# Kernel tuning notes

Hardware: AMD Instinct MI355X
Metric: run time of the kernel (lower is better)

The kernel has to match this reference:

```python
import jax, jax.numpy as jnp
import numpy as np

B = 256
H = W = 14
HW = H * W
TS = 0.03  # sigmoid temperature
TC = 0.07  # contrastive temperature
TP_K = int(HW * 0.1)   # 19
TN_K = int(HW * 0.5)   # 98
EPS_NORM = 1e-12
EPS_PD = 1e-6  # torch F.pairwise_distance eps


def _l2norm(x, axis):
    n = jnp.sqrt(jnp.sum(x * x, axis=axis, keepdims=True))
    return x / jnp.maximum(n, EPS_NORM)


def _conv(x, w):
    return jax.lax.conv_general_dilated(
        x, w, window_strides=(1, 1), padding='SAME',
        dimension_numbers=('NCHW', 'OIHW', 'NCHW'))


def setup_inputs() -> dict:
    key = jax.random.key(0)
    ks = jax.random.split(key, 7)
    ev = jax.random.normal(ks[0], (B, 384, H, W), dtype=jnp.float32)
    ea = jax.random.normal(ks[1], (B, 2048), dtype=jnp.float32)
    masks = jax.random.randint(ks[2], (B, H, W), 0, 2).astype(jnp.int32)
    masks = masks.at[:, 0, 0].set(1)  # guarantee nonzero mask area
    W_fc1 = jax.random.normal(ks[3], (512, 2048), dtype=jnp.float32) * 0.02
    W_fc2 = jax.random.normal(ks[4], (512, 512), dtype=jnp.float32) * 0.02
    W_conv1 = jax.random.normal(ks[5], (512, 384, 3, 3), dtype=jnp.float32) * 0.02
    W_conv2 = jax.random.normal(ks[6], (512, 512, 3, 3), dtype=jnp.float32) * 0.02
    return {'ev': ev, 'ea': ea, 'masks': masks, 'W_fc1': W_fc1,
            'W_fc2': W_fc2, 'W_conv1': W_conv1, 'W_conv2': W_conv2}


def reference(ev, ea, masks, W_fc1, W_fc2, W_conv1, W_conv2):
    # Audio_Proj: fc2(relu(fc1(ea)))  -> (B, 512)
    fa = jnp.maximum(ea @ W_fc1.T, 0.0) @ W_fc2.T

    # Visual_Proj: conv2(relu(conv1(ev))) -> (B, 512, 14, 14)
    fv_map = _conv(jnp.maximum(_conv(ev, W_conv1), 0.0), W_conv2)
    fv_map_norm = _l2norm(fv_map, axis=1)

    # masked mean pooling over the Ncut mask -> indicator vector (B, 512)
    m = masks.astype(jnp.float32)
    ind_vec = jnp.sum(fv_map * m[:, None], axis=(2, 3)) / jnp.sum(m, axis=(1, 2))[:, None]
    ind_vec_norm = _l2norm(ind_vec, axis=1)

    # Sij[i, j, p] = <fv_map_norm[i, :, p], ind_vec_norm[j]>  -> (B, B, HW)
    Sij = jnp.einsum('ichw,jc->ijhw', fv_map_norm, ind_vec_norm).reshape(B, B, HW)

    # per-row topk thresholds (kth largest / kth smallest)
    pos_thr = jax.lax.top_k(Sij, TP_K)[0][..., -1:]           # (B, B, 1)
    neg_thr = -jax.lax.top_k(-Sij, TN_K)[0][..., -1:]         # (B, B, 1)

    m_p = jax.nn.sigmoid((Sij - pos_thr) / TS)
    m_n = 1.0 - jax.nn.sigmoid((Sij - neg_thr) / TS)

    SP = jnp.sum(Sij * m_p, axis=-1) / jnp.sum(m_p, axis=-1)  # (B, B)
    SN = jnp.sum(Sij * m_n, axis=-1) / jnp.sum(m_n, axis=-1)  # (B, B)

    logits1 = jnp.concatenate([SP, SN], axis=1) / TC          # (B, 2B)
    logits2 = jnp.concatenate([SP.T, SN.T], axis=1) / TC
    labels = jnp.arange(B)
    loss1 = -jnp.mean(jax.nn.log_softmax(logits1, axis=-1)[labels, labels])
    loss2 = -jnp.mean(jax.nn.log_softmax(logits2, axis=-1)[labels, labels])

    # squared pairwise distance between detached ind_vec and fa (torch eps in diff)
    diff = jax.lax.stop_gradient(ind_vec)[:, None, :] - fa[None, :, :] + EPS_PD
    dist_mat = jnp.sum(diff * diff, axis=-1)                  # (B, B)

    ivn_d = jax.lax.stop_gradient(ind_vec_norm)
    vv_logits = ivn_d @ ivn_d.T
    eye = jnp.eye(B, dtype=jnp.float32)
    w = -vv_logits * (1.0 - eye) + eye
    dist_mat = dist_mat * w

    mask_mat = eye - (1.0 - eye) / (B - 1)
    loss3 = jnp.mean(jnp.maximum(jnp.sum(dist_mat * mask_mat, axis=1) + 0.6, 0.0))
    loss4 = jnp.mean(jnp.maximum(jnp.sum(dist_mat * mask_mat, axis=0) + 0.6, 0.0))

    return ((loss1 + loss2) / 2.0, (loss3 + loss4) / 2.0)
```

## Files before the change

kernel.cpp:

```cpp
#include <hip/hip_runtime.h>
#include <stdint.h>


typedef __attribute__((ext_vector_type(8))) short bf16x8;
typedef __attribute__((ext_vector_type(4))) short short4v;
typedef __attribute__((ext_vector_type(4))) float f32x4;

__device__ __forceinline__ unsigned short f2bf(float x) {
  unsigned u = __float_as_uint(x);
  unsigned r = u + 0x7FFFu + ((u >> 16) & 1u);
  return (unsigned short)(r >> 16);
}
__device__ __forceinline__ float bf2f(unsigned short h) {
  return __uint_as_float(((unsigned)h) << 16);
}

typedef const __attribute__((address_space(1))) void* gptr1_t;
typedef __attribute__((address_space(3))) void* lptr3_t;
__device__ __forceinline__ void gload_lds16(const void* g, void* l) {
  __builtin_amdgcn_global_load_lds((gptr1_t)g, (lptr3_t)l, 16, 0, 0);
}

__device__ __forceinline__ float waveSum(float v) {
#pragma unroll
  for (int m = 1; m < 64; m <<= 1) v += __shfl_xor(v, m, 64);
  return v;
}
__device__ __forceinline__ float waveMax(float v) {
#pragma unroll
  for (int m = 1; m < 64; m <<= 1) v = fmaxf(v, __shfl_xor(v, m, 64));
  return v;
}
template <int NW>
__device__ __forceinline__ float blockSum(float v) {
  __shared__ float sh[NW];
  v = waveSum(v);
  int wv = threadIdx.x >> 6, ln = threadIdx.x & 63;
  if (ln == 0) sh[wv] = v;
  __syncthreads();
  float r = 0.f;
#pragma unroll
  for (int w = 0; w < NW; ++w) r += sh[w];
  __syncthreads();
  return r;
}
template <int NW>
__device__ __forceinline__ float blockMax(float v) {
  __shared__ float sh[NW];
  v = waveMax(v);
  int wv = threadIdx.x >> 6, ln = threadIdx.x & 63;
  if (ln == 0) sh[wv] = v;
  __syncthreads();
  float r = -3.4e38f;
#pragma unroll
  for (int w = 0; w < NW; ++w) r = fmaxf(r, sh[w]);
  __syncthreads();
  return r;
}

#define RA 65536

template <int KC, int EPI>
__global__ __launch_bounds__(256, 2) void convtap6_k(
    const unsigned short* __restrict__ A, const unsigned short* __restrict__ Bw,
    unsigned short* __restrict__ C) {
  __shared__ __align__(16) short Ah[256 * 72];
  const int tid = threadIdx.x;
  const int wave = tid >> 6, lane = tid & 63;
  const int wm = wave >> 1, wn = wave & 1;
  const int quad = lane >> 4, tq = lane & 15;
  const int img = blockIdx.x, n0 = blockIdx.y * 128;

  int pab[7];
  {
    const int dh = tq >> 3;
    int wq = wm * 8 + (tq & 7);
    if (wq == 0) wq = 8;
    else if (wq == 15) wq = 7;
#pragma unroll
    for (int mi = 0; mi < 7; ++mi) {
      int pr = (1 + 2 * mi + dh) * 16 + wq;
      pab[mi] = (pr - 17) * 144 + quad * 16;
    }
  }
  const int gb = (n0 >> 4) + wn * 4;

  const char* Ab = (const char*)A;
  const char* AhB = (const char*)Ah;
  const int l16 = lane * 16;

  f32x4 acc[7][4];
#pragma unroll
  for (int mi = 0; mi < 7; ++mi)
#pragma unroll
    for (int ni = 0; ni < 4; ++ni) {
      f32x4 z = {0.f, 0.f, 0.f, 0.f};
      acc[mi][ni] = z;
    }

  auto stageA = [&](int kc) {
    size_t s0 = ((size_t)kc * RA + img * 256) * 144;
#pragma unroll
    for (int i = 0; i < 9; ++i) {
      int c = wave + i * 4;
      gload_lds16(Ab + s0 + (size_t)c * 1024 + l16, (char*)Ah + c * 1024);
    }
  };

  stageA(0);
  bf16x8 b0[4], b1[4];
  {
    const size_t w0 = ((size_t)gb * 128 + lane) * 8;
#pragma unroll
    for (int ni = 0; ni < 4; ++ni)
      b0[ni] = *(const bf16x8*)&Bw[w0 + (size_t)ni * 1024];
  }
  __syncthreads();

#pragma unroll 1
  for (int kc = 0; kc < KC; ++kc) {
    const size_t bk = ((size_t)kc * 4096 + gb * 128 + lane) * 8;
#pragma unroll
    for (int t = 0; t < 9; ++t) {
      const size_t tof = (size_t)t * KC * 32768;
#pragma unroll
      for (int ni = 0; ni < 4; ++ni)
        b1[ni] = *(const bf16x8*)&Bw[bk + tof + (size_t)ni * 1024 + 512];
      bf16x8 b0n[4];
      const bool last = (t == 8) && (kc == KC - 1);
      if (!last) {
        const size_t nbase =
            (t < 8) ? bk + (size_t)(t + 1) * KC * 32768 : bk + 32768;
#pragma unroll
        for (int ni = 0; ni < 4; ++ni)
          b0n[ni] = *(const bf16x8*)&Bw[nbase + (size_t)ni * 1024];
      }
      const int OFF = (17 + (t / 3 - 1) * 16 + (t % 3 - 1)) * 144;
      bf16x8 af0[7], af1[7];
#pragma unroll
      for (int mi = 0; mi < 7; ++mi)
        af0[mi] = *(const bf16x8*)(AhB + pab[mi] + OFF);
#pragma unroll
      for (int mi = 0; mi < 7; ++mi)
        af1[mi] = *(const bf16x8*)(AhB + pab[mi] + OFF + 64);
      __builtin_amdgcn_s_setprio(1);
#pragma unroll
      for (int mi = 0; mi < 7; ++mi)
#pragma unroll
        for (int ni = 0; ni < 4; ++ni)
          acc[mi][ni] = __builtin_amdgcn_mfma_f32_16x16x32_bf16(
              af0[mi], b0[ni], acc[mi][ni], 0, 0, 0);
#pragma unroll
      for (int mi = 0; mi < 7; ++mi)
#pragma unroll
        for (int ni = 0; ni < 4; ++ni)
          acc[mi][ni] = __builtin_amdgcn_mfma_f32_16x16x32_bf16(
              af1[mi], b1[ni], acc[mi][ni], 0, 0, 0);
      __builtin_amdgcn_s_setprio(0);
      if (!last) {
#pragma unroll
        for (int ni = 0; ni < 4; ++ni) b0[ni] = b0n[ni];
      }
    }
    if (kc + 1 < KC) {
      __syncthreads();
      stageA(kc + 1);
      __syncthreads();
    }
  }

#pragma unroll
  for (int mi = 0; mi < 7; ++mi) {
#pragma unroll
    for (int r = 0; r < 4; ++r) {
      int idx = quad * 4 + r;
      int wv = wm * 8 + (idx & 7);
      if (wv == 0 || wv == 15) continue;
      int hh = 1 + 2 * mi + (idx >> 3);
      short4v s4;
#pragma unroll
      for (int ni = 0; ni < 4; ++ni) {
        float v = acc[mi][ni][r];
        s4[ni] = (short)f2bf(EPI == 0 ? fmaxf(v, 0.f) : v);
      }
      if (EPI == 0) {
        int cell = img * 256 + hh * 16 + wv;
        int slice = (n0 >> 6) + wn;
        size_t ob = ((size_t)slice * RA + cell) * 72 + tq * 4;
        *(short4v*)&C[ob] = s4;
      } else {
        int p = (hh - 1) * 14 + (wv - 1);
        size_t ob = (size_t)(img * 196 + p) * 512 + n0 + wn * 64 + tq * 4;
        *(short4v*)&C[ob] = s4;
      }
    }
  }
}

template <int K, int NLD, int EPI>
__global__ __launch_bounds__(256, 2) void gemm1_k(
    const unsigned short* __restrict__ A, const unsigned short* __restrict__ Bw,
    void* __restrict__ C, const float* __restrict__ rs) {
  __shared__ short As[2][128 * 64];
  __shared__ short Bs[2][128 * 64];
  const int tid = threadIdx.x;
  const int wave = tid >> 6, lane = tid & 63;
  const int m0 = blockIdx.x * 128, n0 = blockIdx.y * 128;
  const int rr8 = lane >> 3, seg = lane & 7, gseg = seg ^ rr8;
  const int wm = wave >> 1, wn = wave & 1;
  const int quad = lane >> 4, tq = lane & 15;

  size_t asrc[4], bsrc[4];
#pragma unroll
  for (int i8 = 0; i8 < 4; ++i8) {
    int rloc = wave * 32 + i8 * 8 + rr8;
    asrc[i8] = (size_t)(m0 + rloc) * K + gseg * 8;
    bsrc[i8] = (size_t)(n0 + rloc) * K + gseg * 8;
  }

  auto stage = [&](int kc2, int buf) {
    int kb = kc2 * 64;
#pragma unroll
    for (int i8 = 0; i8 < 4; ++i8) {
      gload_lds16(A + asrc[i8] + kb, &As[buf][(wave * 32 + i8 * 8) * 64]);
      gload_lds16(Bw + bsrc[i8] + kb, &Bs[buf][(wave * 32 + i8 * 8) * 64]);
    }
  };

  f32x4 acc[4][4];
#pragma unroll
  for (int mi = 0; mi < 4; ++mi)
#pragma unroll
    for (int ni = 0; ni < 4; ++ni) {
      f32x4 z = {0.f, 0.f, 0.f, 0.f};
      acc[mi][ni] = z;
    }

  const int NK = K / 64;
  stage(0, 0);
  __syncthreads();
#pragma unroll 1
  for (int kc2 = 0; kc2 < NK; ++kc2) {
    const int cur = kc2 & 1;
    if (kc2 + 1 < NK) stage(kc2 + 1, cur ^ 1);
#pragma unroll
    for (int h = 0; h < 2; ++h) {
      bf16x8 af[4], bfr[4];
#pragma unroll
      for (int mi = 0; mi < 4; ++mi) {
        int row = wm * 64 + mi * 16 + tq;
        af[mi] = *(const bf16x8*)&As[cur][row * 64 +
                                         ((((h << 2) | quad) ^ (row & 7)) << 3)];
      }
#pragma unroll
      for (int ni = 0; ni < 4; ++ni) {
        int row = wn * 64 + ni * 16 + tq;
        bfr[ni] = *(const bf16x8*)&Bs[cur][row * 64 +
                                           ((((h << 2) | quad) ^ (row & 7)) << 3)];
      }
#pragma unroll
      for (int mi = 0; mi < 4; ++mi)
#pragma unroll
        for (int ni = 0; ni < 4; ++ni)
          acc[mi][ni] = __builtin_amdgcn_mfma_f32_16x16x32_bf16(
              af[mi], bfr[ni], acc[mi][ni], 0, 0, 0);
    }
    __syncthreads();
  }

#pragma unroll
  for (int mi = 0; mi < 4; ++mi) {
#pragma unroll
    for (int r = 0; r < 4; ++r) {
      int m = m0 + wm * 64 + mi * 16 + quad * 4 + r;
      float sc = (EPI == 3) ? rs[m] : 1.f;
      size_t obase = (size_t)m * NLD + n0 + wn * 64 + tq;
#pragma unroll
      for (int ni = 0; ni < 4; ++ni) {
        float v = acc[mi][ni][r];
        size_t idx = obase + ni * 16;
        if (EPI == 0)
          ((unsigned short*)C)[idx] = f2bf(fmaxf(v, 0.f));
        else if (EPI == 2)
          ((float*)C)[idx] = v;
        else
          ((float*)C)[idx] = v * sc;
      }
    }
  }
}

__global__ __launch_bounds__(256, 2) void gemm_xv_k(
    const unsigned short* __restrict__ ivpb, const unsigned short* __restrict__ fab,
    const unsigned short* __restrict__ indnb, float* __restrict__ Xm,
    float* __restrict__ Vm) {
  const unsigned short* A = blockIdx.z ? indnb : ivpb;
  const unsigned short* Bw = blockIdx.z ? indnb : fab;
  float* C = blockIdx.z ? Vm : Xm;
  __shared__ short As[2][128 * 64];
  __shared__ short Bs[2][128 * 64];
  const int tid = threadIdx.x;
  const int wave = tid >> 6, lane = tid & 63;
  const int m0 = blockIdx.x * 128, n0 = blockIdx.y * 128;
  const int rr8 = lane >> 3, seg = lane & 7, gseg = seg ^ rr8;
  const int wm = wave >> 1, wn = wave & 1;
  const int quad = lane >> 4, tq = lane & 15;
  size_t asrc[4], bsrc[4];
#pragma unroll
  for (int i8 = 0; i8 < 4; ++i8) {
    int rloc = wave * 32 + i8 * 8 + rr8;
    asrc[i8] = (size_t)(m0 + rloc) * 512 + gseg * 8;
    bsrc[i8] = (size_t)(n0 + rloc) * 512 + gseg * 8;
  }
  auto stage = [&](int kc2, int buf) {
    int kb = kc2 * 64;
#pragma unroll
    for (int i8 = 0; i8 < 4; ++i8) {
      gload_lds16(A + asrc[i8] + kb, &As[buf][(wave * 32 + i8 * 8) * 64]);
      gload_lds16(Bw + bsrc[i8] + kb, &Bs[buf][(wave * 32 + i8 * 8) * 64]);
    }
  };
  f32x4 acc[4][4];
#pragma unroll
  for (int mi = 0; mi < 4; ++mi)
#pragma unroll
    for (int ni = 0; ni < 4; ++ni) {
      f32x4 z = {0.f, 0.f, 0.f, 0.f};
      acc[mi][ni] = z;
    }
  stage(0, 0);
  __syncthreads();
#pragma unroll 1
  for (int kc2 = 0; kc2 < 8; ++kc2) {
    const int cur = kc2 & 1;
    if (kc2 + 1 < 8) stage(kc2 + 1, cur ^ 1);
#pragma unroll
    for (int h = 0; h < 2; ++h) {
      bf16x8 af[4], bfr[4];
#pragma unroll
      for (int mi = 0; mi < 4; ++mi) {
        int row = wm * 64 + mi * 16 + tq;
        af[mi] = *(const bf16x8*)&As[cur][row * 64 +
                                         ((((h << 2) | quad) ^ (row & 7)) << 3)];
      }
#pragma unroll
      for (int ni = 0; ni < 4; ++ni) {
        int row = wn * 64 + ni * 16 + tq;
        bfr[ni] = *(const bf16x8*)&Bs[cur][row * 64 +
                                           ((((h << 2) | quad) ^ (row & 7)) << 3)];
      }
#pragma unroll
      for (int mi = 0; mi < 4; ++mi)
#pragma unroll
        for (int ni = 0; ni < 4; ++ni)
          acc[mi][ni] = __builtin_amdgcn_mfma_f32_16x16x32_bf16(
              af[mi], bfr[ni], acc[mi][ni], 0, 0, 0);
    }
    __syncthreads();
  }
#pragma unroll
  for (int mi = 0; mi < 4; ++mi)
#pragma unroll
    for (int r = 0; r < 4; ++r) {
      int m = m0 + wm * 64 + mi * 16 + quad * 4 + r;
      size_t obase = (size_t)m * 256 + n0 + wn * 64 + tq;
#pragma unroll
      for (int ni = 0; ni < 4; ++ni) C[obase + ni * 16] = acc[mi][ni][r];
    }
}

__global__ void prep_all_k(const float* __restrict__ ea,
                           const float* __restrict__ Wf1,
                           const float* __restrict__ Wf2,
                           const float* __restrict__ Wc1,
                           const float* __restrict__ Wc2,
                           unsigned short* __restrict__ eab,
                           unsigned short* __restrict__ wf1b,
                           unsigned short* __restrict__ wf2b,
                           unsigned short* __restrict__ wb1,
                           unsigned short* __restrict__ wb2,
                           unsigned int* __restrict__ x1u) {
  int i = blockIdx.x * 256 + threadIdx.x;
  if (i < 524288) {
    eab[i] = f2bf(ea[i]);
  } else if (i < 1572864) {
    int j = i - 524288;
    wf1b[j] = f2bf(Wf1[j]);
  } else if (i < 1835008) {
    int j = i - 1572864;
    wf2b[j] = f2bf(Wf2[j]);
  } else if (i < 3604480) {
    int j = i - 1835008;
    int t = j / (6 * 32768), r = j - t * (6 * 32768);
    int kc = r / 32768, r2 = r - kc * 32768;
    int g = r2 >> 10, h = (r2 >> 9) & 1, quad = (r2 >> 7) & 3;
    int tq = (r2 >> 3) & 15, jj = r2 & 7;
    int n = g * 16 + tq, cin = kc * 64 + h * 32 + quad * 8 + jj;
    wb1[j] = f2bf(Wc1[(n * 384 + cin) * 9 + t]);
  } else if (i < 5963776) {
    int j = i - 3604480;
    int t = j / (8 * 32768), r = j - t * (8 * 32768);
    int kc = r / 32768, r2 = r - kc * 32768;
    int g = r2 >> 10, h = (r2 >> 9) & 1, quad = (r2 >> 7) & 3;
    int tq = (r2 >> 3) & 15, jj = r2 & 7;
    int n = g * 16 + tq;
    int cin = kc * 64 + (jj & 3) * 16 + h * 8 + quad * 2 + (jj >> 2);
    wb2[j] = f2bf(Wc2[(n * 512 + cin) * 9 + t]);
  } else {
    int j = i - 5963776;
    int hr = j >> 8, u = j & 255;
    int slice = u >> 5, uu = u & 31;
    int b = hr / 60, c = hr - b * 60;
    int cell;
    if (c < 16) cell = c;
    else if (c < 32) cell = 240 + (c - 16);
    else if (c < 46) cell = (c - 31) * 16;
    else cell = (c - 45) * 16 + 15;
    x1u[((size_t)slice * RA + b * 256 + cell) * 36 + uu] = 0u;
  }
}

__global__ __launch_bounds__(256) void evpad_k(const float* __restrict__ ev,
                                               unsigned short* __restrict__ out) {
  int b = blockIdx.x, ct = blockIdx.y;
  __shared__ float tile[64][197];
  int tid = threadIdx.x;
  const float* src = ev + ((size_t)b * 384 + ct * 64) * 196;
#pragma unroll 1
  for (int it = 0; it < 49; ++it) {
    int idx = it * 256 + tid;
    int c = idx / 196, p = idx - c * 196;
    tile[c][p] = src[idx];
  }
  __syncthreads();
  unsigned short* dst = out + ((size_t)ct * RA + b * 256) * 72;
#pragma unroll 1
  for (int it = 0; it < 64; ++it) {
    int idx = it * 256 + tid;
    int cell = idx >> 6, c = idx & 63;
    int h = (cell >> 4) - 1, w = (cell & 15) - 1;
    float v = ((unsigned)h < 14u && (unsigned)w < 14u) ? tile[c][h * 14 + w]
                                                       : 0.f;
    dst[(size_t)cell * 72 + c] = f2bf(v);
  }
}

__global__ __launch_bounds__(512) void poolfa_k(
    const unsigned short* __restrict__ fv, const int* __restrict__ masks,
    const float* __restrict__ fa, unsigned short* __restrict__ indnb,
    unsigned short* __restrict__ ivpb, unsigned short* __restrict__ fab,
    float* __restrict__ Pi, float* __restrict__ Qj, float* __restrict__ rn) {
  int bid = blockIdx.x;
  int tid = threadIdx.x;
  if (bid >= 256) {
    int b = bid - 256;
    int s64 = tid & 63;
    int chan = (tid & ~63) | ((s64 & 3) * 16 + (s64 >> 2));
    float v = fa[b * 512 + chan];
    fab[b * 512 + tid] = f2bf(v);
    float q = blockSum<8>(v * v);
    if (tid == 0) Qj[b] = q;
    return;
  }
  int b = bid;
  int w = tid >> 6, lane = tid & 63;
  __shared__ float red[8][512];
  __shared__ float msh[8];
  float acc[8] = {0.f, 0.f, 0.f, 0.f, 0.f, 0.f, 0.f, 0.f};
  float msum = 0.f;
  for (int p = w; p < 196; p += 8) {
    float m = (float)masks[b * 196 + p];
    msum += m;
    uint4 d = *(const uint4*)(fv + (size_t)(b * 196 + p) * 512 + lane * 8);
    const unsigned short* hp = (const unsigned short*)&d;
    float ss = 0.f;
#pragma unroll
    for (int k = 0; k < 8; ++k) {
      float x = bf2f(hp[k]);
      ss += x * x;
      acc[k] += m * x;
    }
    ss = waveSum(ss);
    if (lane == 0) rn[b * 196 + p] = 1.f / fmaxf(sqrtf(ss), 1e-12f);
  }
#pragma unroll
  for (int k = 0; k < 8; ++k) red[w][lane * 8 + k] = acc[k];
  if (lane == 0) msh[w] = msum;
  __syncthreads();
  float s = 0.f, mtot = 0.f;
#pragma unroll
  for (int ww = 0; ww < 8; ++ww) {
    s += red[ww][tid];
    mtot += msh[ww];
  }
  float v = s / mtot;
  float ss2 = blockSum<8>(v * v);
  float sc = 1.f / fmaxf(sqrtf(ss2), 1e-12f);
  indnb[b * 512 + tid] = f2bf(v * sc);
  float ve = v + 1e-6f;
  ivpb[b * 512 + tid] = f2bf(ve);
  float p2 = blockSum<8>(ve * ve);
  if (tid == 0) Pi[b] = p2;
}


__device__ __forceinline__ float radix_kth(unsigned k0, unsigned k1, unsigned k2,
                                           unsigned k3, int k) {
  unsigned prefix = 0;
  int kk = k;
#pragma unroll 1
  for (int bit = 31; bit >= 14; --bit) {
    unsigned thi = (prefix >> bit) | 1u;
    int c = __popcll(__ballot((k0 >> bit) == thi)) +
            __popcll(__ballot((k1 >> bit) == thi)) +
            __popcll(__ballot((k2 >> bit) == thi)) +
            __popcll(__ballot((k3 >> bit) == thi));
    if (kk <= c)
      prefix |= (1u << bit);
    else
      kk -= c;
  }
  unsigned u = (prefix & 0x80000000u) ? (prefix ^ 0x80000000u) : ~prefix;
  return __uint_as_float(u);
}
__device__ __forceinline__ unsigned sortkey(float x) {
  unsigned u = __float_as_uint(x);
  return u ^ (((int)u >> 31) | 0x80000000u);
}

__global__ __launch_bounds__(256) void spsn_k(const float* __restrict__ Sij,
                                              float* __restrict__ SP,
                                              float* __restrict__ SN) {
  int i = blockIdx.x, jg = blockIdx.y;
  int tid = threadIdx.x, wave = tid >> 6, lane = tid & 63;
  __shared__ float tile[196 * 65];
#pragma unroll 1
  for (int it = 0; it < 49; ++it) {
    int lin = it * 256 + tid;
    int p = lin >> 6, j = lin & 63;
    tile[p * 65 + j] = Sij[(size_t)(i * 196 + p) * 256 + jg * 64 + j];
  }
  __syncthreads();
#pragma unroll 1
  for (int jj = 0; jj < 16; ++jj) {
    int j = jj * 4 + wave;
    float v0 = tile[lane * 65 + j];
    float v1 = tile[(lane + 64) * 65 + j];
    float v2 = tile[(lane + 128) * 65 + j];
    bool val3 = lane < 4;
    float v3 = val3 ? tile[(lane + 192) * 65 + j] : 0.f;
    unsigned k0 = sortkey(v0), k1 = sortkey(v1), k2 = sortkey(v2);
    unsigned k3 = val3 ? sortkey(v3) : 0u;
    float thrP = radix_kth(k0, k1, k2, k3, 19);
    float thrN = radix_kth(k0, k1, k2, k3, 99);
    float spn = 0.f, spd = 0.f, snn = 0.f, snd = 0.f;
    const float invTS = 1.f / 0.03f;
#pragma unroll
    for (int q = 0; q < 4; ++q) {
      float v = (q == 0) ? v0 : (q == 1) ? v1 : (q == 2) ? v2 : v3;
      bool ok = (q < 3) || val3;
      if (ok) {
        float mp = 1.f / (1.f + __expf((thrP - v) * invTS));
        float mn = 1.f / (1.f + __expf((v - thrN) * invTS));
        spn += v * mp;
        spd += mp;
        snn += v * mn;
        snd += mn;
      }
    }
    spn = waveSum(spn); spd = waveSum(spd);
    snn = waveSum(snn); snd = waveSum(snd);
    if (lane == 0) {
      SP[i * 256 + jg * 64 + j] = spn / spd;
      SN[i * 256 + jg * 64 + j] = snn / snd;
    }
  }
}

__global__ __launch_bounds__(256) void lossA_k(
    const float* __restrict__ SP, const float* __restrict__ SN,
    const float* __restrict__ Pi, const float* __restrict__ Qj,
    const float* __restrict__ X, const float* __restrict__ V,
    float* __restrict__ val, float* __restrict__ out) {
  int r = blockIdx.x;
  int tid = threadIdx.x;
  if (r < 512) {
    int i = r & 255;
    bool col = r >= 256;
    const float invTC = 1.f / 0.07f;
    float a = (col ? SP[tid * 256 + i] : SP[i * 256 + tid]) * invTC;
    float b = (col ? SN[tid * 256 + i] : SN[i * 256 + tid]) * invTC;
    float mx = blockMax<4>(fmaxf(a, b));
    float se = blockSum<4>(__expf(a - mx) + __expf(b - mx));
    float lse = mx + __logf(se);
    if (tid == 0) {
      float diag = SP[i * 256 + i] * invTC;
      atomicAdd(out, -(diag - lse) * (1.f / 512.f));
    }
  } else {
    int i = r - 512, j = tid;
    float d = Pi[i] - 2.f * X[i * 256 + j] + Qj[j];
    float w = (i == j) ? 1.f : -V[i * 256 + j];
    float x = d * w;
    val[i * 256 + j] = x;
    __shared__ float diag_sh;
    if (j == i) diag_sh = x;
    float tot = blockSum<4>(x);
    if (j == 0) {
      float rs = diag_sh - (tot - diag_sh) * (1.f / 255.f);
      atomicAdd(out + 1, fmaxf(rs + 0.6f, 0.f) * (1.f / 512.f));
    }
  }
}

__global__ __launch_bounds__(256) void loss4_k(const float* __restrict__ val,
                                               float* __restrict__ out) {
  int j = blockIdx.x, i = threadIdx.x;
  float x = val[i * 256 + j];
  __shared__ float diag_sh;
  if (i == j) diag_sh = x;
  float tot = blockSum<4>(x);
  if (i == 0) {
    float cs = diag_sh - (tot - diag_sh) * (1.f / 255.f);
    atomicAdd(out + 1, fmaxf(cs + 0.6f, 0.f) * (1.f / 512.f));
  }
}


extern "C" void kernel_launch(void* const* d_in, const int* in_sizes, int n_in,
                              void* d_out, int out_size, void* d_ws,
                              size_t ws_size, hipStream_t stream) {
  (void)in_sizes; (void)n_in; (void)out_size; (void)ws_size;
  const float* ev = (const float*)d_in[0];
  const float* ea = (const float*)d_in[1];
  const int* msk = (const int*)d_in[2];
  const float* Wf1 = (const float*)d_in[3];
  const float* Wf2 = (const float*)d_in[4];
  const float* Wc1 = (const float*)d_in[5];
  const float* Wc2 = (const float*)d_in[6];
  float* out = (float*)d_out;
  char* ws = (char*)d_ws;

  size_t off = 0;
  auto alloc = [&](size_t bytes) {
    void* p = ws + off;
    off = (off + bytes + 255) & ~(size_t)255;
    return p;
  };
  unsigned short* evb = (unsigned short*)alloc((size_t)6 * RA * 144);
  unsigned short* fv = evb;
  unsigned short* x1b = (unsigned short*)alloc((size_t)8 * RA * 144);
  float* Sij = (float*)x1b;
  unsigned short* wb1 = (unsigned short*)alloc((size_t)9 * 6 * 32768 * 2);
  unsigned short* wb2 = (unsigned short*)alloc((size_t)9 * 8 * 32768 * 2);
  unsigned short* eab = (unsigned short*)alloc((size_t)256 * 2048 * 2);
  unsigned short* wf1b = (unsigned short*)alloc((size_t)512 * 2048 * 2);
  unsigned short* wf2b = (unsigned short*)alloc((size_t)512 * 512 * 2);
  unsigned short* hb = (unsigned short*)alloc((size_t)256 * 512 * 2);
  float* fa = (float*)alloc((size_t)256 * 512 * 4);
  unsigned short* indnb = (unsigned short*)alloc((size_t)256 * 512 * 2);
  unsigned short* ivpb = (unsigned short*)alloc((size_t)256 * 512 * 2);
  unsigned short* fab = (unsigned short*)alloc((size_t)256 * 512 * 2);
  float* Pi = (float*)alloc(256 * 4);
  float* Qj = (float*)alloc(256 * 4);
  float* Xm = (float*)alloc((size_t)256 * 256 * 4);
  float* Vm = (float*)alloc((size_t)256 * 256 * 4);
  float* rn = (float*)alloc((size_t)50176 * 4);
  float* SP = (float*)alloc((size_t)256 * 256 * 4);
  float* SN = (float*)alloc((size_t)256 * 256 * 4);
  float* val = (float*)alloc((size_t)256 * 256 * 4);

  hipMemsetAsync(out, 0, 2 * sizeof(float), stream);

  prep_all_k<<<38656, 256, 0, stream>>>(ea, Wf1, Wf2, Wc1, Wc2, eab, wf1b,
                                        wf2b, wb1, wb2, (unsigned int*)x1b);
  evpad_k<<<dim3(256, 6), 256, 0, stream>>>(ev, evb);

  convtap6_k<6, 0><<<dim3(256, 4), 256, 0, stream>>>(evb, wb1, x1b);
  gemm1_k<2048, 512, 0><<<dim3(2, 4), 256, 0, stream>>>(eab, wf1b, hb, nullptr);
  gemm1_k<512, 512, 2><<<dim3(2, 4), 256, 0, stream>>>(hb, wf2b, fa, nullptr);
  convtap6_k<8, 1><<<dim3(256, 4), 256, 0, stream>>>(x1b, wb2, fv);

  poolfa_k<<<512, 512, 0, stream>>>(fv, msk, fa, indnb, ivpb, fab, Pi, Qj, rn);

  gemm1_k<512, 256, 3><<<dim3(392, 2), 256, 0, stream>>>(fv, indnb, Sij, rn);
  gemm_xv_k<<<dim3(2, 2, 2), 256, 0, stream>>>(ivpb, fab, indnb, Xm, Vm);

  spsn_k<<<dim3(256, 4), 256, 0, stream>>>(Sij, SP, SN);
  lossA_k<<<768, 256, 0, stream>>>(SP, SN, Pi, Qj, Xm, Vm, val, out);
  loss4_k<<<256, 256, 0, stream>>>(val, out);
}
```

Before: 767.8 us.

## Fuse Sij GEMM into top-k soft-mask kernel to skip Sij round trip

Replaces the separate Sij GEMM and SP/SN kernel with one kernel. Each block computes its 196x64 slice of Sij with bf16 MFMA from the padded feature map, staged into LDS with a swizzle. It then applies the row norm scaling and runs the radix top-k and soft-mask sums straight from LDS. This removes the 51 MB fp32 Sij write and read-back and one launch. The trade-off is that each block recomputes its A-tile load, with 4 blocks per image reading the same fv slice, and the GEMM runs at lower occupancy inside a heavy LDS kernel.

```diff
diff --git a/kernel.cpp b/kernel.cpp
--- a/kernel.cpp
+++ b/kernel.cpp
@@ -528,27 +528,117 @@
   return u ^ (((int)u >> 31) | 0x80000000u);
 }
 
-__global__ __launch_bounds__(256) void spsn_k(const float* __restrict__ Sij,
-                                              float* __restrict__ SP,
-                                              float* __restrict__ SN) {
-  int i = blockIdx.x, jg = blockIdx.y;
-  int tid = threadIdx.x, wave = tid >> 6, lane = tid & 63;
-  __shared__ float tile[196 * 65];
+__global__ __launch_bounds__(256) void sijspsn_k(
+    const unsigned short* __restrict__ fv, const unsigned short* __restrict__ indnb,
+    const float* __restrict__ rn, float* __restrict__ SP,
+    float* __restrict__ SN) {
+  __shared__ __align__(16) float tile[196 * 65];
+  char* AhB = (char*)tile;
+  const int tid = threadIdx.x;
+  const int wave = tid >> 6, lane = tid & 63;
+  const int wm = wave >> 1, wn = wave & 1;
+  const int quad = lane >> 4, tq = lane & 15;
+  const int img = blockIdx.x, jg = blockIdx.y;
+
+  int prow[7];
+  {
+    const int dh = tq >> 3;
+    int wq = wm * 8 + (tq & 7);
+    if (wq == 0) wq = 8;
+    else if (wq == 15) wq = 7;
+#pragma unroll
+    for (int mi = 0; mi < 7; ++mi) {
+      int hh = 1 + 2 * mi + dh;
+      prow[mi] = (hh - 1) * 14 + (wq - 1);
+    }
+  }
+
+  f32x4 acc[7][2];
+#pragma unroll
+  for (int mi = 0; mi < 7; ++mi)
+#pragma unroll
+    for (int ni = 0; ni < 2; ++ni) {
+      f32x4 z = {0.f, 0.f, 0.f, 0.f};
+      acc[mi][ni] = z;
+    }
+
+  const int rloc = lane >> 3, sseg = lane & 7;
+  const int sxor = sseg ^ rloc;
+  auto stageA = [&](int kc) {
+#pragma unroll
+    for (int it = 0; it < 7; ++it) {
+      int c = wave + it * 4;
+      const unsigned short* src =
+          fv + ((size_t)(img * 196 + c * 8 + rloc)) * 512 + kc * 64 + sxor * 8;
+      gload_lds16(src, AhB + c * 1024 + lane * 16);
+    }
+  };
+
 #pragma unroll 1
-  for (int it = 0; it < 49; ++it) {
-    int lin = it * 256 + tid;
-    int p = lin >> 6, j = lin & 63;
-    tile[p * 65 + j] = Sij[(size_t)(i * 196 + p) * 256 + jg * 64 + j];
-  }
-  __syncthreads();
+  for (int kc = 0; kc < 8; ++kc) {
+    __syncthreads();
+    stageA(kc);
+    bf16x8 bfr[2][2];
+#pragma unroll
+    for (int ni = 0; ni < 2; ++ni)
+#pragma unroll
+      for (int h = 0; h < 2; ++h) {
+        int n = jg * 64 + wn * 32 + ni * 16 + tq;
+        bfr[ni][h] = *(const bf16x8*)&indnb[(size_t)n * 512 + kc * 64 +
+                                            h * 32 + quad * 8];
+      }
+    __syncthreads();
+    __builtin_amdgcn_s_setprio(1);
+#pragma unroll
+    for (int h = 0; h < 2; ++h) {
+      bf16x8 af[7];
+#pragma unroll
+      for (int mi = 0; mi < 7; ++mi) {
+        int p = prow[mi];
+        int seg = (h * 4 + quad) ^ (p & 7);
+        af[mi] = *(const bf16x8*)(AhB + p * 128 + seg * 16);
+      }
+#pragma unroll
+      for (int mi = 0; mi < 7; ++mi)
+#pragma unroll
+        for (int ni = 0; ni < 2; ++ni)
+          acc[mi][ni] = __builtin_amdgcn_mfma_f32_16x16x32_bf16(
+              af[mi], bfr[ni][h], acc[mi][ni], 0, 0, 0);
+    }
+    __builtin_amdgcn_s_setprio(0);
+  }
+  __syncthreads();
+
+#pragma unroll
+  for (int mi = 0; mi < 7; ++mi) {
+#pragma unroll
+    for (int r = 0; r < 4; ++r) {
+      int idx = quad * 4 + r;
+      int wv = wm * 8 + (idx & 7);
+      if (wv == 0 || wv == 15) continue;
+      int hh = 1 + 2 * mi + (idx >> 3);
+      int p = (hh - 1) * 14 + (wv - 1);
+#pragma unroll
+      for (int ni = 0; ni < 2; ++ni) {
+        int jl = wn * 32 + ni * 16 + tq;
+        tile[p * 65 + jl] = acc[mi][ni][r];
+      }
+    }
+  }
+  __syncthreads();
+
+  const float rn0 = rn[img * 196 + lane];
+  const float rn1 = rn[img * 196 + lane + 64];
+  const float rn2 = rn[img * 196 + lane + 128];
+  const bool val3 = lane < 4;
+  const float rn3 = val3 ? rn[img * 196 + lane + 192] : 0.f;
 #pragma unroll 1
   for (int jj = 0; jj < 16; ++jj) {
     int j = jj * 4 + wave;
-    float v0 = tile[lane * 65 + j];
-    float v1 = tile[(lane + 64) * 65 + j];
-    float v2 = tile[(lane + 128) * 65 + j];
-    bool val3 = lane < 4;
-    float v3 = val3 ? tile[(lane + 192) * 65 + j] : 0.f;
+    float v0 = tile[lane * 65 + j] * rn0;
+    float v1 = tile[(lane + 64) * 65 + j] * rn1;
+    float v2 = tile[(lane + 128) * 65 + j] * rn2;
+    float v3 = val3 ? tile[(lane + 192) * 65 + j] * rn3 : 0.f;
     unsigned k0 = sortkey(v0), k1 = sortkey(v1), k2 = sortkey(v2);
     unsigned k3 = val3 ? sortkey(v3) : 0u;
     float thrP = radix_kth(k0, k1, k2, k3, 19);
@@ -571,8 +661,8 @@
     spn = waveSum(spn); spd = waveSum(spd);
     snn = waveSum(snn); snd = waveSum(snd);
     if (lane == 0) {
-      SP[i * 256 + jg * 64 + j] = spn / spd;
-      SN[i * 256 + jg * 64 + j] = snn / snd;
+      SP[img * 256 + jg * 64 + j] = spn / spd;
+      SN[img * 256 + jg * 64 + j] = snn / snd;
     }
   }
 }
@@ -650,7 +740,6 @@
   unsigned short* evb = (unsigned short*)alloc((size_t)6 * RA * 144);
   unsigned short* fv = evb;
   unsigned short* x1b = (unsigned short*)alloc((size_t)8 * RA * 144);
-  float* Sij = (float*)x1b;
   unsigned short* wb1 = (unsigned short*)alloc((size_t)9 * 6 * 32768 * 2);
   unsigned short* wb2 = (unsigned short*)alloc((size_t)9 * 8 * 32768 * 2);
   unsigned short* eab = (unsigned short*)alloc((size_t)256 * 2048 * 2);
@@ -683,10 +772,9 @@
 
   poolfa_k<<<512, 512, 0, stream>>>(fv, msk, fa, indnb, ivpb, fab, Pi, Qj, rn);
 
-  gemm1_k<512, 256, 3><<<dim3(392, 2), 256, 0, stream>>>(fv, indnb, Sij, rn);
+  sijspsn_k<<<dim3(256, 4), 256, 0, stream>>>(fv, indnb, rn, SP, SN);
   gemm_xv_k<<<dim3(2, 2, 2), 256, 0, stream>>>(ivpb, fab, indnb, Xm, Vm);
 
-  spsn_k<<<dim3(256, 4), 256, 0, stream>>>(Sij, SP, SN);
   lossA_k<<<768, 256, 0, stream>>>(SP, SN, Pi, Qj, Xm, Vm, val, out);
   loss4_k<<<256, 256, 0, stream>>>(val, out);
 }
```

After: 791.5 us. 1.03x slower.

## Merge small launches: fold evpad into prep, XV gemm into spsn, loss4 into lossF

Applied to the files above, without the earlier changes.

Combines the ev padding conversion with the weight/input bf16 prep kernel, runs the small X/V GEMMs as extra blocks of the SP/SN top-k kernel, and folds the column-wise loss4 reduction into the loss kernel by recomputing values instead of storing them. The aim is to cut kernel launch count and gaps between tiny kernels and to drop the val buffer round trip. In exchange, the fused GEMM loses its double buffering and shares the large LDS tile allocation, and the loss blocks recompute distances.

```diff
diff --git a/kernel.cpp b/kernel.cpp
--- a/kernel.cpp
+++ b/kernel.cpp
@@ -290,97 +290,41 @@
   }
 }
 
-__global__ __launch_bounds__(256, 2) void gemm_xv_k(
-    const unsigned short* __restrict__ ivpb, const unsigned short* __restrict__ fab,
-    const unsigned short* __restrict__ indnb, float* __restrict__ Xm,
-    float* __restrict__ Vm) {
-  const unsigned short* A = blockIdx.z ? indnb : ivpb;
-  const unsigned short* Bw = blockIdx.z ? indnb : fab;
-  float* C = blockIdx.z ? Vm : Xm;
-  __shared__ short As[2][128 * 64];
-  __shared__ short Bs[2][128 * 64];
+__global__ __launch_bounds__(256) void prepev_k(
+    const float* __restrict__ ea, const float* __restrict__ Wf1,
+    const float* __restrict__ Wf2, const float* __restrict__ Wc1,
+    const float* __restrict__ Wc2, const float* __restrict__ ev,
+    unsigned short* __restrict__ eab, unsigned short* __restrict__ wf1b,
+    unsigned short* __restrict__ wf2b, unsigned short* __restrict__ wb1,
+    unsigned short* __restrict__ wb2, unsigned int* __restrict__ x1u,
+    unsigned short* __restrict__ evb) {
+  __shared__ float tile[64][197];
+  const int blk = blockIdx.x;
   const int tid = threadIdx.x;
-  const int wave = tid >> 6, lane = tid & 63;
-  const int m0 = blockIdx.x * 128, n0 = blockIdx.y * 128;
-  const int rr8 = lane >> 3, seg = lane & 7, gseg = seg ^ rr8;
-  const int wm = wave >> 1, wn = wave & 1;
-  const int quad = lane >> 4, tq = lane & 15;
-  size_t asrc[4], bsrc[4];
-#pragma unroll
-  for (int i8 = 0; i8 < 4; ++i8) {
-    int rloc = wave * 32 + i8 * 8 + rr8;
-    asrc[i8] = (size_t)(m0 + rloc) * 512 + gseg * 8;
-    bsrc[i8] = (size_t)(n0 + rloc) * 512 + gseg * 8;
-  }
-  auto stage = [&](int kc2, int buf) {
-    int kb = kc2 * 64;
-#pragma unroll
-    for (int i8 = 0; i8 < 4; ++i8) {
-      gload_lds16(A + asrc[i8] + kb, &As[buf][(wave * 32 + i8 * 8) * 64]);
-      gload_lds16(Bw + bsrc[i8] + kb, &Bs[buf][(wave * 32 + i8 * 8) * 64]);
-    }
-  };
-  f32x4 acc[4][4];
-#pragma unroll
-  for (int mi = 0; mi < 4; ++mi)
-#pragma unroll
-    for (int ni = 0; ni < 4; ++ni) {
-      f32x4 z = {0.f, 0.f, 0.f, 0.f};
-      acc[mi][ni] = z;
-    }
-  stage(0, 0);
-  __syncthreads();
-#pragma unroll 1
-  for (int kc2 = 0; kc2 < 8; ++kc2) {
-    const int cur = kc2 & 1;
-    if (kc2 + 1 < 8) stage(kc2 + 1, cur ^ 1);
-#pragma unroll
-    for (int h = 0; h < 2; ++h) {
-      bf16x8 af[4], bfr[4];
-#pragma unroll
-      for (int mi = 0; mi < 4; ++mi) {
-        int row = wm * 64 + mi * 16 + tq;
-        af[mi] = *(const bf16x8*)&As[cur][row * 64 +
-                                         ((((h << 2) | quad) ^ (row & 7)) << 3)];
-      }
-#pragma unroll
-      for (int ni = 0; ni < 4; ++ni) {
-        int row = wn * 64 + ni * 16 + tq;
-        bfr[ni] = *(const bf16x8*)&Bs[cur][row * 64 +
-                                           ((((h << 2) | quad) ^ (row & 7)) << 3)];
-      }
-#pragma unroll
-      for (int mi = 0; mi < 4; ++mi)
-#pragma unroll
-        for (int ni = 0; ni < 4; ++ni)
-          acc[mi][ni] = __builtin_amdgcn_mfma_f32_16x16x32_bf16(
-              af[mi], bfr[ni], acc[mi][ni], 0, 0, 0);
+  if (blk >= 38656) {
+    int ep = blk - 38656;
+    int b = ep & 255, ct = ep >> 8;
+    const float* src = ev + ((size_t)b * 384 + ct * 64) * 196;
+#pragma unroll 1
+    for (int it = 0; it < 49; ++it) {
+      int idx = it * 256 + tid;
+      int c = idx / 196, p = idx - c * 196;
+      tile[c][p] = src[idx];
     }
     __syncthreads();
-  }
-#pragma unroll
-  for (int mi = 0; mi < 4; ++mi)
-#pragma unroll
-    for (int r = 0; r < 4; ++r) {
-      int m = m0 + wm * 64 + mi * 16 + quad * 4 + r;
-      size_t obase = (size_t)m * 256 + n0 + wn * 64 + tq;
-#pragma unroll
-      for (int ni = 0; ni < 4; ++ni) C[obase + ni * 16] = acc[mi][ni][r];
-    }
-}
-
-__global__ void prep_all_k(const float* __restrict__ ea,
-                           const float* __restrict__ Wf1,
-                           const float* __restrict__ Wf2,
-                           const float* __restrict__ Wc1,
-                           const float* __restrict__ Wc2,
-                           unsigned short* __restrict__ eab,
-                           unsigned short* __restrict__ wf1b,
-                           unsigned short* __restrict__ wf2b,
-                           unsigned short* __restrict__ wb1,
-                           unsigned short* __restrict__ wb2,
-                           unsigned int* __restrict__ x1u) {
-  int i = blockIdx.x * 256 + threadIdx.x;
+    unsigned short* dst = evb + ((size_t)ct * RA + b * 256) * 72;
+#pragma unroll 1
+    for (int it = 0; it < 64; ++it) {
+      int idx = it * 256 + tid;
+      int cell = idx >> 6, c = idx & 63;
+      int h = (cell >> 4) - 1, w = (cell & 15) - 1;
+      float v = ((unsigned)h < 14u && (unsigned)w < 14u) ? tile[c][h * 14 + w]
+                                                         : 0.f;
+      dst[(size_t)cell * 72 + c] = f2bf(v);
+    }
+    return;
+  }
+  int i = blk * 256 + tid;
   if (i < 524288) {
     eab[i] = f2bf(ea[i]);
   } else if (i < 1572864) {
@@ -420,31 +364,6 @@
   }
 }
 
-__global__ __launch_bounds__(256) void evpad_k(const float* __restrict__ ev,
-                                               unsigned short* __restrict__ out) {
-  int b = blockIdx.x, ct = blockIdx.y;
-  __shared__ float tile[64][197];
-  int tid = threadIdx.x;
-  const float* src = ev + ((size_t)b * 384 + ct * 64) * 196;
-#pragma unroll 1
-  for (int it = 0; it < 49; ++it) {
-    int idx = it * 256 + tid;
-    int c = idx / 196, p = idx - c * 196;
-    tile[c][p] = src[idx];
-  }
-  __syncthreads();
-  unsigned short* dst = out + ((size_t)ct * RA + b * 256) * 72;
-#pragma unroll 1
-  for (int it = 0; it < 64; ++it) {
-    int idx = it * 256 + tid;
-    int cell = idx >> 6, c = idx & 63;
-    int h = (cell >> 4) - 1, w = (cell & 15) - 1;
-    float v = ((unsigned)h < 14u && (unsigned)w < 14u) ? tile[c][h * 14 + w]
-                                                       : 0.f;
-    dst[(size_t)cell * 72 + c] = f2bf(v);
-  }
-}
-
 __global__ __launch_bounds__(512) void poolfa_k(
     const unsigned short* __restrict__ fv, const int* __restrict__ masks,
     const float* __restrict__ fa, unsigned short* __restrict__ indnb,
@@ -528,12 +447,91 @@
   return u ^ (((int)u >> 31) | 0x80000000u);
 }
 
-__global__ __launch_bounds__(256) void spsn_k(const float* __restrict__ Sij,
-                                              float* __restrict__ SP,
-                                              float* __restrict__ SN) {
-  int i = blockIdx.x, jg = blockIdx.y;
-  int tid = threadIdx.x, wave = tid >> 6, lane = tid & 63;
-  __shared__ float tile[196 * 65];
+__global__ __launch_bounds__(256) void spsnxv_k(
+    const float* __restrict__ Sij, const float* __restrict__ rn,
+    const unsigned short* __restrict__ ivpb,
+    const unsigned short* __restrict__ fab,
+    const unsigned short* __restrict__ indnb, float* __restrict__ SP,
+    float* __restrict__ SN, float* __restrict__ Xm, float* __restrict__ Vm) {
+  __shared__ __align__(16) float tile[196 * 65];
+  const int tid = threadIdx.x;
+  const int flat = blockIdx.x;
+  const int wave = tid >> 6, lane = tid & 63;
+
+  if (flat >= 1024) {
+    int g = flat - 1024;
+    const unsigned short* A = (g >> 2) ? indnb : ivpb;
+    const unsigned short* Bw = (g >> 2) ? indnb : fab;
+    float* C = (g >> 2) ? Vm : Xm;
+    const int m0 = (g & 1) * 128, n0 = ((g >> 1) & 1) * 128;
+    short* As = (short*)tile;
+    short* Bs = As + 128 * 64;
+    const int rr8 = lane >> 3, seg = lane & 7, gseg = seg ^ rr8;
+    const int wm = wave >> 1, wn = wave & 1;
+    const int quad = lane >> 4, tq = lane & 15;
+    size_t asrc[4], bsrc[4];
+#pragma unroll
+    for (int i8 = 0; i8 < 4; ++i8) {
+      int rloc = wave * 32 + i8 * 8 + rr8;
+      asrc[i8] = (size_t)(m0 + rloc) * 512 + gseg * 8;
+      bsrc[i8] = (size_t)(n0 + rloc) * 512 + gseg * 8;
+    }
+    f32x4 acc[4][4];
+#pragma unroll
+    for (int mi = 0; mi < 4; ++mi)
+#pragma unroll
+      for (int ni = 0; ni < 4; ++ni) {
+        f32x4 z = {0.f, 0.f, 0.f, 0.f};
+        acc[mi][ni] = z;
+      }
+#pragma unroll 1
+    for (int kc2 = 0; kc2 < 8; ++kc2) {
+      int kb = kc2 * 64;
+      __syncthreads();
+#pragma unroll
+      for (int i8 = 0; i8 < 4; ++i8) {
+        gload_lds16(A + asrc[i8] + kb, &As[(wave * 32 + i8 * 8) * 64]);
+        gload_lds16(Bw + bsrc[i8] + kb, &Bs[(wave * 32 + i8 * 8) * 64]);
+      }
+      __syncthreads();
+#pragma unroll
+      for (int h = 0; h < 2; ++h) {
+        bf16x8 af[4], bfr[4];
+#pragma unroll
+        for (int mi = 0; mi < 4; ++mi) {
+          int row = wm * 64 + mi * 16 + tq;
+          af[mi] = *(const bf16x8*)&As[row * 64 +
+                                       ((((h << 2) | quad) ^ (row & 7)) << 3)];
+        }
+#pragma unroll
+        for (int ni = 0; ni < 4; ++ni) {
+          int row = wn * 64 + ni * 16 + tq;
+          bfr[ni] = *(const bf16x8*)&Bs[row * 64 +
+                                        ((((h << 2) | quad) ^ (row & 7)) << 3)];
+        }
+#pragma unroll
+        for (int mi = 0; mi < 4; ++mi)
+#pragma unroll
+          for (int ni = 0; ni < 4; ++ni)
+            acc[mi][ni] = __builtin_amdgcn_mfma_f32_16x16x32_bf16(
+                af[mi], bfr[ni], acc[mi][ni], 0, 0, 0);
+      }
+    }
+    const int wm2 = wave >> 1, wn2 = wave & 1;
+    const int quad2 = lane >> 4, tq2 = lane & 15;
+#pragma unroll
+    for (int mi = 0; mi < 4; ++mi)
+#pragma unroll
+      for (int r = 0; r < 4; ++r) {
+        int m = m0 + wm2 * 64 + mi * 16 + quad2 * 4 + r;
+        size_t obase = (size_t)m * 256 + n0 + wn2 * 64 + tq2;
+#pragma unroll
+        for (int ni = 0; ni < 4; ++ni) C[obase + ni * 16] = acc[mi][ni][r];
+      }
+    return;
+  }
+
+  const int i = flat & 255, jg = flat >> 8;
 #pragma unroll 1
   for (int it = 0; it < 49; ++it) {
     int lin = it * 256 + tid;
@@ -577,11 +575,11 @@
   }
 }
 
-__global__ __launch_bounds__(256) void lossA_k(
+__global__ __launch_bounds__(256) void lossF_k(
     const float* __restrict__ SP, const float* __restrict__ SN,
     const float* __restrict__ Pi, const float* __restrict__ Qj,
     const float* __restrict__ X, const float* __restrict__ V,
-    float* __restrict__ val, float* __restrict__ out) {
+    float* __restrict__ out) {
   int r = blockIdx.x;
   int tid = threadIdx.x;
   if (r < 512) {
@@ -597,12 +595,11 @@
       float diag = SP[i * 256 + i] * invTC;
       atomicAdd(out, -(diag - lse) * (1.f / 512.f));
     }
-  } else {
+  } else if (r < 768) {
     int i = r - 512, j = tid;
     float d = Pi[i] - 2.f * X[i * 256 + j] + Qj[j];
     float w = (i == j) ? 1.f : -V[i * 256 + j];
     float x = d * w;
-    val[i * 256 + j] = x;
     __shared__ float diag_sh;
     if (j == i) diag_sh = x;
     float tot = blockSum<4>(x);
@@ -610,19 +607,18 @@
       float rs = diag_sh - (tot - diag_sh) * (1.f / 255.f);
       atomicAdd(out + 1, fmaxf(rs + 0.6f, 0.f) * (1.f / 512.f));
     }
-  }
-}
-
-__global__ __launch_bounds__(256) void loss4_k(const float* __restrict__ val,
-                                               float* __restrict__ out) {
-  int j = blockIdx.x, i = threadIdx.x;
-  float x = val[i * 256 + j];
-  __shared__ float diag_sh;
-  if (i == j) diag_sh = x;
-  float tot = blockSum<4>(x);
-  if (i == 0) {
-    float cs = diag_sh - (tot - diag_sh) * (1.f / 255.f);
-    atomicAdd(out + 1, fmaxf(cs + 0.6f, 0.f) * (1.f / 512.f));
+  } else {
+    int j = r - 768, i = tid;
+    float d = Pi[i] - 2.f * X[i * 256 + j] + Qj[j];
+    float w = (i == j) ? 1.f : -V[i * 256 + j];
+    float x = d * w;
+    __shared__ float diag_sh;
+    if (i == j) diag_sh = x;
+    float tot = blockSum<4>(x);
+    if (i == 0) {
+      float cs = diag_sh - (tot - diag_sh) * (1.f / 255.f);
+      atomicAdd(out + 1, fmaxf(cs + 0.6f, 0.f) * (1.f / 512.f));
+    }
   }
 }
 
@@ -668,13 +664,11 @@
   float* rn = (float*)alloc((size_t)50176 * 4);
   float* SP = (float*)alloc((size_t)256 * 256 * 4);
   float* SN = (float*)alloc((size_t)256 * 256 * 4);
-  float* val = (float*)alloc((size_t)256 * 256 * 4);
 
   hipMemsetAsync(out, 0, 2 * sizeof(float), stream);
 
-  prep_all_k<<<38656, 256, 0, stream>>>(ea, Wf1, Wf2, Wc1, Wc2, eab, wf1b,
-                                        wf2b, wb1, wb2, (unsigned int*)x1b);
-  evpad_k<<<dim3(256, 6), 256, 0, stream>>>(ev, evb);
+  prepev_k<<<40192, 256, 0, stream>>>(ea, Wf1, Wf2, Wc1, Wc2, ev, eab, wf1b,
+                                      wf2b, wb1, wb2, (unsigned int*)x1b, evb);
 
   convtap6_k<6, 0><<<dim3(256, 4), 256, 0, stream>>>(evb, wb1, x1b);
   gemm1_k<2048, 512, 0><<<dim3(2, 4), 256, 0, stream>>>(eab, wf1b, hb, nullptr);
@@ -684,9 +678,8 @@
   poolfa_k<<<512, 512, 0, stream>>>(fv, msk, fa, indnb, ivpb, fab, Pi, Qj, rn);
 
   gemm1_k<512, 256, 3><<<dim3(392, 2), 256, 0, stream>>>(fv, indnb, Sij, rn);
-  gemm_xv_k<<<dim3(2, 2, 2), 256, 0, stream>>>(ivpb, fab, indnb, Xm, Vm);
-
-  spsn_k<<<dim3(256, 4), 256, 0, stream>>>(Sij, SP, SN);
-  lossA_k<<<768, 256, 0, stream>>>(SP, SN, Pi, Qj, Xm, Vm, val, out);
-  loss4_k<<<256, 256, 0, stream>>>(val, out);
-}
+
+  spsnxv_k<<<1032, 256, 0, stream>>>(Sij, rn, ivpb, fab, indnb, SP, SN, Xm, Vm);
+
+  lossF_k<<<1024, 256, 0, stream>>>(SP, SN, Pi, Qj, Xm, Vm, out);
+}
```

Result: no change. 778.4 us (+1.4%).
